# Optimization experiments

Hardware: AMD Instinct MI355X
Metric: run time of the kernel (lower is better)

## Reference

```python
import jax, jax.numpy as jnp
import numpy as np

N_NODES = 100000
N_EDGES = 1600000
IN_FEATS = 128
N_HIDDEN = 128
N_CLASSES = 40
EPS = 1e-12  # torch F.normalize eps


def _sage_conv(h, src, dst, W_self, b_self, W_neigh, b_neigh, act, norm):
    # mean aggregation over in-neighbors: dst receives from src
    agg = jax.ops.segment_sum(h[src], dst, num_segments=N_NODES)  # [N, D]
    deg = jax.ops.segment_sum(jnp.ones(dst.shape, h.dtype), dst, num_segments=N_NODES)
    h_neigh = agg / jnp.maximum(deg, 1.0)[:, None]
    out = h @ W_self + b_self + h_neigh @ W_neigh + b_neigh
    if act:
        out = jax.nn.relu(out)
    if norm:
        out = out / jnp.maximum(
            jnp.linalg.norm(out, axis=1, keepdims=True), EPS)
    return out


def setup_inputs() -> dict:
    key = jax.random.key(0)
    ks = jax.random.split(key, 16)
    def lin(k, fan_in, fan_out):
        s = 1.0 / np.sqrt(fan_in)
        return jax.random.uniform(k, (fan_in, fan_out), jnp.float32, -s, s)
    inp = {
        "features": jax.random.normal(ks[0], (N_NODES, IN_FEATS), jnp.float32),
        "src": jax.random.randint(ks[1], (N_EDGES,), 0, N_NODES, jnp.int32),
        "dst": jax.random.randint(ks[2], (N_EDGES,), 0, N_NODES, jnp.int32),
        # layer 0: in -> hidden
        "Ws0": lin(ks[3], IN_FEATS, N_HIDDEN), "bs0": jnp.zeros((N_HIDDEN,), jnp.float32),
        "Wn0": lin(ks[4], IN_FEATS, N_HIDDEN), "bn0": jnp.zeros((N_HIDDEN,), jnp.float32),
        # layer 1: hidden -> hidden
        "Ws1": lin(ks[5], N_HIDDEN, N_HIDDEN), "bs1": jnp.zeros((N_HIDDEN,), jnp.float32),
        "Wn1": lin(ks[6], N_HIDDEN, N_HIDDEN), "bn1": jnp.zeros((N_HIDDEN,), jnp.float32),
        # layer 2: hidden -> classes (no activation, no norm)
        "Ws2": lin(ks[7], N_HIDDEN, N_CLASSES), "bs2": jnp.zeros((N_CLASSES,), jnp.float32),
        "Wn2": lin(ks[8], N_HIDDEN, N_CLASSES), "bn2": jnp.zeros((N_CLASSES,), jnp.float32),
    }
    return inp


def reference(features, src, dst,
              Ws0, bs0, Wn0, bn0,
              Ws1, bs1, Wn1, bn1,
              Ws2, bs2, Wn2, bn2):
    h = _sage_conv(features, src, dst, Ws0, bs0, Wn0, bn0, act=True, norm=True)
    h = _sage_conv(h, src, dst, Ws1, bs1, Wn1, bn1, act=True, norm=True)
    out = _sage_conv(h, src, dst, Ws2, bs2, Wn2, bn2, act=False, norm=False)
    return out
```

## Files before the change

kernel.cpp:

```cpp
#include <hip/hip_runtime.h>
#include <hip/hip_bf16.h>

#define N_NODES_C 100000
#define N_EDGES_C 1600000
#define N_BUCK ((N_NODES_C + 255) / 256)
#define BCAP 4608
#define PART_NB 160
#define PART_CHUNK ((N_EDGES_C + PART_NB - 1) / PART_NB)

typedef __attribute__((ext_vector_type(8))) short          short8;
typedef __attribute__((ext_vector_type(4))) float          f32x4;
typedef __attribute__((ext_vector_type(4))) unsigned int   u32x4;
typedef __attribute__((ext_vector_type(4))) unsigned short u16x4;

__device__ inline float load1v(const void* p, size_t i, int bf) {
    return bf ? __bfloat162float(((const __hip_bfloat16*)p)[i])
              : ((const float*)p)[i];
}
__device__ inline unsigned short f2bf(float f) {
    __hip_bfloat16 h = __float2bfloat16(f);
    return *reinterpret_cast<unsigned short*>(&h);
}
__device__ inline float bf_lo(unsigned u) { return __uint_as_float(u << 16); }
__device__ inline float bf_hi(unsigned u) { return __uint_as_float(u & 0xffff0000u); }
__device__ inline void acc8(float* a, u32x4 r) {
    a[0] += bf_lo(r.x); a[1] += bf_hi(r.x);
    a[2] += bf_lo(r.y); a[3] += bf_hi(r.y);
    a[4] += bf_lo(r.z); a[5] += bf_hi(r.z);
    a[6] += bf_lo(r.w); a[7] += bf_hi(r.w);
}

__global__ void detect_init(const void* __restrict__ feats, int* __restrict__ gflag,
                            int* __restrict__ bcur) {
    const unsigned short* u = (const unsigned short*)feats;
    int bad = 0;
    for (int i = threadIdx.x; i < 2048; i += 64) {
        unsigned e = (u[i] >> 7) & 0xFF;
        if (e >= 0xC0) bad++;
    }
#pragma unroll
    for (int off = 32; off > 0; off >>= 1) bad += __shfl_down(bad, off, 64);
    if (threadIdx.x == 0) *gflag = (bad == 0) ? 1 : 0;
    for (int b = threadIdx.x; b < N_BUCK; b += 64) bcur[b] = b * BCAP;
}

__global__ __launch_bounds__(256) void partition2(
        const int* __restrict__ src, const int* __restrict__ dst,
        int* __restrict__ bcur, unsigned* __restrict__ pairs) {
    __shared__ int cnt[N_BUCK];
    __shared__ int lbase[N_BUCK];
    int tid = threadIdx.x;
    int e0 = blockIdx.x * PART_CHUNK;
    int e1 = min(e0 + PART_CHUNK, N_EDGES_C);
    for (int i = tid; i < N_BUCK; i += 256) cnt[i] = 0;
    __syncthreads();
    for (int e = e0 + tid; e < e1; e += 256)
        atomicAdd(&cnt[dst[e] >> 8], 1);
    __syncthreads();
    for (int i = tid; i < N_BUCK; i += 256) {
        int c = cnt[i];
        lbase[i] = c ? atomicAdd(&bcur[i], c) : 0;
        cnt[i] = 0;
    }
    __syncthreads();
    for (int e = e0 + tid; e < e1; e += 256) {
        int s = src[e], d = dst[e];
        int bk = d >> 8;
        int pos = lbase[bk] + atomicAdd(&cnt[bk], 1);
        pairs[pos] = ((unsigned)(d & 255) << 17) | (unsigned)s;
    }
}

__global__ __launch_bounds__(256) void bucket_fill(
        const unsigned* __restrict__ pairs, const int* __restrict__ bcur,
        int* __restrict__ csr, int* __restrict__ row_start, int* __restrict__ deg) {
    __shared__ int cnt[256], sd[256], lcur[256];
    int b = blockIdx.x, tid = threadIdx.x;
    int pbase = b * BCAP;

    int psum = 0;
    for (int i = tid; i < b; i += 256) psum += bcur[i] - i * BCAP;
    sd[tid] = psum;
    __syncthreads();
    for (int st = 128; st > 0; st >>= 1) {
        if (tid < st) sd[tid] += sd[tid + st];
        __syncthreads();
    }
    int base = sd[0];
    int count = bcur[b] - b * BCAP;

    cnt[tid] = 0;
    __syncthreads();
    for (int i = tid; i < count; i += 256)
        atomicAdd(&cnt[pairs[pbase + i] >> 17], 1);
    __syncthreads();
    sd[tid] = cnt[tid];
    __syncthreads();
    for (int st = 1; st < 256; st <<= 1) {
        int t = (tid >= st) ? sd[tid - st] : 0;
        __syncthreads();
        sd[tid] += t;
        __syncthreads();
    }
    int excl = sd[tid] - cnt[tid];
    int node = b * 256 + tid;
    if (node < N_NODES_C) { row_start[node] = base + excl; deg[node] = cnt[tid]; }
    lcur[tid] = excl;
    __syncthreads();
    for (int i = tid; i < count; i += 256) {
        unsigned p = pairs[pbase + i];
        int pos = base + atomicAdd(&lcur[p >> 17], 1);
        csr[pos] = (int)(p & 0x1FFFFu);
    }
}

__global__ void prep_weights(const void* Ws0, const void* bs0, const void* Wn0, const void* bn0,
                             const void* Ws1, const void* bs1, const void* Wn1, const void* bn1,
                             const void* Ws2, const void* bs2, const void* Wn2, const void* bn2,
                             unsigned short* __restrict__ Wt, float* __restrict__ bcat,
                             const int* __restrict__ gflag) {
    int gb = *gflag;
    int n = blockIdx.x;
    int k = threadIdx.x;
    if (n < 128) {
        float v = (k < 128) ? load1v(Ws0, (size_t)k * 128 + n, gb)
                            : load1v(Wn0, (size_t)(k - 128) * 128 + n, gb);
        Wt[(size_t)n * 256 + k] = f2bf(v);
        if (k == 0) bcat[n] = load1v(bs0, n, gb) + load1v(bn0, n, gb);
    } else if (n < 256) {
        int c = n - 128;
        float v = (k < 128) ? load1v(Ws1, (size_t)k * 128 + c, gb)
                            : load1v(Wn1, (size_t)(k - 128) * 128 + c, gb);
        Wt[(size_t)n * 256 + k] = f2bf(v);
        if (k == 0) bcat[n] = load1v(bs1, c, gb) + load1v(bn1, c, gb);
    } else {
        int c = n - 256;
        if (k < 128) {
            float v = (c < 40) ? load1v(Ws2, (size_t)k * 40 + c, gb)
                               : load1v(Wn2, (size_t)k * 40 + (c - 40), gb);
            Wt[65536 + (size_t)c * 128 + k] = f2bf(v);
        }
        if (k == 0) bcat[n] = (c < 40) ? load1v(bs2, c, gb) + load1v(bn2, c, gb) : 0.0f;
    }
}

__global__ __launch_bounds__(256) void gather_kernel(
        const void* __restrict__ hsrc, int src_stride,
        int src_mode, int copy_self,
        const int* __restrict__ csr,
        const int* __restrict__ row_start,
        const int* __restrict__ deg,
        unsigned short* __restrict__ X,
        const int* __restrict__ gflag) {
    int wave = threadIdx.x >> 6, lane = threadIdx.x & 63;
    int g = lane >> 4, sub = lane & 15;
    int srcLane = lane & 48;
    int node = blockIdx.x * 16 + wave * 4 + g;
    bool valid = node < N_NODES_C;
    int vnode = valid ? node : (N_NODES_C - 1);
    int start = row_start[vnode];
    int d = valid ? deg[vnode] : 0;
    const int* cp = csr + start;
    float inv = (d > 0) ? 1.0f / (float)d : 0.0f;
    int bf = (src_mode == 2) ? *gflag : src_mode;

    if (bf) {
        const unsigned short* hb = (const unsigned short*)hsrc;
        float a[8] = {0, 0, 0, 0, 0, 0, 0, 0};
        for (int base = 0; base < d; base += 16) {
            int n16 = min(d - base, 16);
            int idxr = cp[base + ((sub < n16) ? sub : 0)];
            int i = 0;
            for (; i + 8 <= n16; i += 8) {
                int nb0 = __shfl(idxr, srcLane + i + 0, 64);
                int nb1 = __shfl(idxr, srcLane + i + 1, 64);
                int nb2 = __shfl(idxr, srcLane + i + 2, 64);
                int nb3 = __shfl(idxr, srcLane + i + 3, 64);
                int nb4 = __shfl(idxr, srcLane + i + 4, 64);
                int nb5 = __shfl(idxr, srcLane + i + 5, 64);
                int nb6 = __shfl(idxr, srcLane + i + 6, 64);
                int nb7 = __shfl(idxr, srcLane + i + 7, 64);
                u32x4 r0 = *(const u32x4*)(hb + (size_t)nb0 * src_stride + sub * 8);
                u32x4 r1 = *(const u32x4*)(hb + (size_t)nb1 * src_stride + sub * 8);
                u32x4 r2 = *(const u32x4*)(hb + (size_t)nb2 * src_stride + sub * 8);
                u32x4 r3 = *(const u32x4*)(hb + (size_t)nb3 * src_stride + sub * 8);
                u32x4 r4 = *(const u32x4*)(hb + (size_t)nb4 * src_stride + sub * 8);
                u32x4 r5 = *(const u32x4*)(hb + (size_t)nb5 * src_stride + sub * 8);
                u32x4 r6 = *(const u32x4*)(hb + (size_t)nb6 * src_stride + sub * 8);
                u32x4 r7 = *(const u32x4*)(hb + (size_t)nb7 * src_stride + sub * 8);
                acc8(a, r0); acc8(a, r1); acc8(a, r2); acc8(a, r3);
                acc8(a, r4); acc8(a, r5); acc8(a, r6); acc8(a, r7);
            }
            for (; i + 4 <= n16; i += 4) {
                int nb0 = __shfl(idxr, srcLane + i + 0, 64);
                int nb1 = __shfl(idxr, srcLane + i + 1, 64);
                int nb2 = __shfl(idxr, srcLane + i + 2, 64);
                int nb3 = __shfl(idxr, srcLane + i + 3, 64);
                u32x4 r0 = *(const u32x4*)(hb + (size_t)nb0 * src_stride + sub * 8);
                u32x4 r1 = *(const u32x4*)(hb + (size_t)nb1 * src_stride + sub * 8);
                u32x4 r2 = *(const u32x4*)(hb + (size_t)nb2 * src_stride + sub * 8);
                u32x4 r3 = *(const u32x4*)(hb + (size_t)nb3 * src_stride + sub * 8);
                acc8(a, r0); acc8(a, r1); acc8(a, r2); acc8(a, r3);
            }
            for (; i < n16; ++i) {
                int nb = __shfl(idxr, srcLane + i, 64);
                u32x4 r = *(const u32x4*)(hb + (size_t)nb * src_stride + sub * 8);
                acc8(a, r);
            }
        }
        if (valid) {
            u32x4 o;
            o.x = (unsigned)f2bf(a[0] * inv) | ((unsigned)f2bf(a[1] * inv) << 16);
            o.y = (unsigned)f2bf(a[2] * inv) | ((unsigned)f2bf(a[3] * inv) << 16);
            o.z = (unsigned)f2bf(a[4] * inv) | ((unsigned)f2bf(a[5] * inv) << 16);
            o.w = (unsigned)f2bf(a[6] * inv) | ((unsigned)f2bf(a[7] * inv) << 16);
            *(u32x4*)(X + (size_t)node * 256 + 128 + sub * 8) = o;
            if (copy_self) {
                u32x4 raw = *(const u32x4*)(hb + (size_t)node * src_stride + sub * 8);
                *(u32x4*)(X + (size_t)node * 256 + sub * 8) = raw;
            }
        }
    } else {
        const float* hf = (const float*)hsrc;
        float a[8] = {0, 0, 0, 0, 0, 0, 0, 0};
        for (int base = 0; base < d; base += 16) {
            int n16 = min(d - base, 16);
            int idxr = cp[base + ((sub < n16) ? sub : 0)];
            int i = 0;
            for (; i + 4 <= n16; i += 4) {
                int nb0 = __shfl(idxr, srcLane + i + 0, 64);
                int nb1 = __shfl(idxr, srcLane + i + 1, 64);
                int nb2 = __shfl(idxr, srcLane + i + 2, 64);
                int nb3 = __shfl(idxr, srcLane + i + 3, 64);
                const float* p0 = hf + (size_t)nb0 * src_stride + sub * 4;
                const float* p1 = hf + (size_t)nb1 * src_stride + sub * 4;
                const float* p2 = hf + (size_t)nb2 * src_stride + sub * 4;
                const float* p3 = hf + (size_t)nb3 * src_stride + sub * 4;
                f32x4 a0 = *(const f32x4*)p0, b0 = *(const f32x4*)(p0 + 64);
                f32x4 a1 = *(const f32x4*)p1, b1 = *(const f32x4*)(p1 + 64);
                f32x4 a2 = *(const f32x4*)p2, b2 = *(const f32x4*)(p2 + 64);
                f32x4 a3 = *(const f32x4*)p3, b3 = *(const f32x4*)(p3 + 64);
#pragma unroll
                for (int k = 0; k < 4; ++k) {
                    a[k] += a0[k] + a1[k] + a2[k] + a3[k];
                    a[4 + k] += b0[k] + b1[k] + b2[k] + b3[k];
                }
            }
            for (; i < n16; ++i) {
                int nb = __shfl(idxr, srcLane + i, 64);
                const float* p0 = hf + (size_t)nb * src_stride + sub * 4;
                f32x4 a0 = *(const f32x4*)p0, b0 = *(const f32x4*)(p0 + 64);
#pragma unroll
                for (int k = 0; k < 4; ++k) { a[k] += a0[k]; a[4 + k] += b0[k]; }
            }
        }
        if (valid) {
            u16x4 oa = { f2bf(a[0] * inv), f2bf(a[1] * inv),
                         f2bf(a[2] * inv), f2bf(a[3] * inv) };
            u16x4 ob = { f2bf(a[4] * inv), f2bf(a[5] * inv),
                         f2bf(a[6] * inv), f2bf(a[7] * inv) };
            *(u16x4*)(X + (size_t)node * 256 + 128 + sub * 4) = oa;
            *(u16x4*)(X + (size_t)node * 256 + 128 + 64 + sub * 4) = ob;
            if (copy_self) {
                const float* sp = hf + (size_t)node * src_stride + sub * 4;
                f32x4 ra = *(const f32x4*)sp;
                f32x4 rb = *(const f32x4*)(sp + 64);
                u16x4 sa = { f2bf(ra.x), f2bf(ra.y), f2bf(ra.z), f2bf(ra.w) };
                u16x4 sb = { f2bf(rb.x), f2bf(rb.y), f2bf(rb.z), f2bf(rb.w) };
                *(u16x4*)(X + (size_t)node * 256 + sub * 4) = sa;
                *(u16x4*)(X + (size_t)node * 256 + 64 + sub * 4) = sb;
            }
        }
    }
}

template <int NCT, int KT, int CHK, bool ACTNORM, bool DUAL>
__global__ __launch_bounds__(256) void mfma_gemm(
        const unsigned short* __restrict__ X, int astride,
        const u32x4* __restrict__ Wg,
        const float* __restrict__ bias,
        unsigned short* __restrict__ out, int out_stride,
        unsigned short* __restrict__ Ybuf, unsigned short* __restrict__ Zbuf,
        int n_nodes) {
    __shared__ u32x4 ldsW[NCT * 16 * CHK];
    int tid = threadIdx.x;
    for (int c = tid; c < NCT * 16 * CHK; c += 256) {
        int nrow = c / CHK, ch = c % CHK;
        ldsW[nrow * CHK + (ch ^ (nrow & 7))] = Wg[c];
    }
    __syncthreads();

    int wave = tid >> 6, lane = tid & 63;
    int quad = lane >> 4, sub = lane & 15;
    int mynode = blockIdx.x * 64 + wave * 16 + sub;
    int arow = (mynode < n_nodes) ? mynode : (n_nodes - 1);
    const unsigned short* ap = X + (size_t)arow * astride + quad * 8;

    f32x4 acc[NCT];
#pragma unroll
    for (int ct = 0; ct < NCT; ++ct) acc[ct] = (f32x4){0,0,0,0};

    short8 av = *(const short8*)ap;
#pragma unroll
    for (int kt = 0; kt < KT; ++kt) {
        short8 av_next = av;
        if (kt < KT - 1) av_next = *(const short8*)(ap + (kt + 1) * 32);
        int chunk = kt * 4 + quad;
#pragma unroll
        for (int ct = 0; ct < NCT; ++ct) {
            int ncol = ct * 16 + sub;
            union { u32x4 u; short8 s; } cv;
            cv.u = ldsW[ncol * CHK + (chunk ^ (ncol & 7))];
            acc[ct] = __builtin_amdgcn_mfma_f32_16x16x32_bf16(cv.s, av, acc[ct], 0, 0, 0);
        }
        av = av_next;
    }

    float ss = 0.0f;
#pragma unroll
    for (int ct = 0; ct < NCT; ++ct) {
        f32x4 b4 = *(const f32x4*)(bias + ct * 16 + quad * 4);
#pragma unroll
        for (int r = 0; r < 4; ++r) {
            float v = acc[ct][r] + b4[r];
            if (ACTNORM) { v = fmaxf(v, 0.0f); ss += v * v; }
            acc[ct][r] = v;
        }
    }
    float scale = 1.0f;
    if (ACTNORM) {
        ss += __shfl_xor(ss, 16, 64);
        ss += __shfl_xor(ss, 32, 64);
        scale = 1.0f / fmaxf(sqrtf(ss), 1e-12f);
    }
    if (mynode < n_nodes) {
#pragma unroll
        for (int ct = 0; ct < NCT; ++ct) {
            int c0 = ct * 16 + quad * 4;
            u16x4 o = { f2bf(acc[ct][0] * scale), f2bf(acc[ct][1] * scale),
                        f2bf(acc[ct][2] * scale), f2bf(acc[ct][3] * scale) };
            if (DUAL) {
                if (c0 < 40) *(u16x4*)(Zbuf + (size_t)mynode * 64 + c0) = o;
                else         *(u16x4*)(Ybuf + (size_t)mynode * 64 + (c0 - 40)) = o;
            } else {
                *(u16x4*)(out + (size_t)mynode * out_stride + c0) = o;
            }
        }
    }
}

__global__ __launch_bounds__(256) void combine_kernel(
        const unsigned short* __restrict__ Y2,
        const unsigned short* __restrict__ Z2,
        const int* __restrict__ csr,
        const int* __restrict__ row_start,
        const int* __restrict__ deg,
        void* __restrict__ out,
        const int* __restrict__ gflag) {
    int wave = threadIdx.x >> 6, lane = threadIdx.x & 63;
    int grp = lane >> 3, sub = lane & 7;
    int grpLane = lane & 56;
    int node = blockIdx.x * 32 + wave * 8 + grp;
    bool valid = node < N_NODES_C;
    int vnode = valid ? node : (N_NODES_C - 1);
    int start = row_start[vnode];
    int d = valid ? deg[vnode] : 0;
    const int* cp = csr + start;

    float a[8] = {0, 0, 0, 0, 0, 0, 0, 0};
    for (int base = 0; base < d; base += 8) {
        int n8 = min(d - base, 8);
        int idxr = cp[base + ((sub < n8) ? sub : 0)];
        if (n8 == 8) {
            int nb0 = __shfl(idxr, grpLane + 0, 64);
            int nb1 = __shfl(idxr, grpLane + 1, 64);
            int nb2 = __shfl(idxr, grpLane + 2, 64);
            int nb3 = __shfl(idxr, grpLane + 3, 64);
            int nb4 = __shfl(idxr, grpLane + 4, 64);
            int nb5 = __shfl(idxr, grpLane + 5, 64);
            int nb6 = __shfl(idxr, grpLane + 6, 64);
            int nb7 = __shfl(idxr, grpLane + 7, 64);
            u32x4 r0 = *(const u32x4*)(Y2 + (size_t)nb0 * 64 + sub * 8);
            u32x4 r1 = *(const u32x4*)(Y2 + (size_t)nb1 * 64 + sub * 8);
            u32x4 r2 = *(const u32x4*)(Y2 + (size_t)nb2 * 64 + sub * 8);
            u32x4 r3 = *(const u32x4*)(Y2 + (size_t)nb3 * 64 + sub * 8);
            u32x4 r4 = *(const u32x4*)(Y2 + (size_t)nb4 * 64 + sub * 8);
            u32x4 r5 = *(const u32x4*)(Y2 + (size_t)nb5 * 64 + sub * 8);
            u32x4 r6 = *(const u32x4*)(Y2 + (size_t)nb6 * 64 + sub * 8);
            u32x4 r7 = *(const u32x4*)(Y2 + (size_t)nb7 * 64 + sub * 8);
            acc8(a, r0); acc8(a, r1); acc8(a, r2); acc8(a, r3);
            acc8(a, r4); acc8(a, r5); acc8(a, r6); acc8(a, r7);
        } else {
            for (int j = 0; j < n8; ++j) {
                int nb = __shfl(idxr, grpLane + j, 64);
                u32x4 r = *(const u32x4*)(Y2 + (size_t)nb * 64 + sub * 8);
                acc8(a, r);
            }
        }
    }

    if (valid) {
        float inv = (d > 0) ? 1.0f / (float)d : 0.0f;
        u32x4 z = *(const u32x4*)(Z2 + (size_t)node * 64 + sub * 8);
        float v[8];
        v[0] = a[0] * inv + bf_lo(z.x); v[1] = a[1] * inv + bf_hi(z.x);
        v[2] = a[2] * inv + bf_lo(z.y); v[3] = a[3] * inv + bf_hi(z.y);
        v[4] = a[4] * inv + bf_lo(z.z); v[5] = a[5] * inv + bf_hi(z.z);
        v[6] = a[6] * inv + bf_lo(z.w); v[7] = a[7] * inv + bf_hi(z.w);
        if (sub < 5) {
            if (*gflag) {
                u32x4 o;
                o.x = (unsigned)f2bf(v[0]) | ((unsigned)f2bf(v[1]) << 16);
                o.y = (unsigned)f2bf(v[2]) | ((unsigned)f2bf(v[3]) << 16);
                o.z = (unsigned)f2bf(v[4]) | ((unsigned)f2bf(v[5]) << 16);
                o.w = (unsigned)f2bf(v[6]) | ((unsigned)f2bf(v[7]) << 16);
                *(u32x4*)((unsigned short*)out + (size_t)node * 40 + sub * 8) = o;
            } else {
                float* op = (float*)out + (size_t)node * 40 + sub * 8;
                f32x4 o0 = { v[0], v[1], v[2], v[3] };
                f32x4 o1 = { v[4], v[5], v[6], v[7] };
                *(f32x4*)op = o0;
                *(f32x4*)(op + 4) = o1;
            }
        }
    }
}

extern "C" void kernel_launch(void* const* d_in, const int* in_sizes, int n_in,
                              void* d_out, int out_size, void* d_ws, size_t ws_size,
                              hipStream_t stream) {
    const void* feats = d_in[0];
    const int*  src   = (const int*)d_in[1];
    const int*  dst   = (const int*)d_in[2];

    char* ws = (char*)d_ws;
    unsigned short* X0   = (unsigned short*)ws;
    unsigned short* X1   = (unsigned short*)(ws + 51200000);
    unsigned short* Wt   = (unsigned short*)(ws + 102400000);
    float*          bcat = (float*)(ws + 102912000);
    unsigned short* Y2   = (unsigned short*)(ws + 102916096);
    unsigned short* Z2   = (unsigned short*)(ws + 115716096);
    unsigned*       pairs= (unsigned*)(ws + 102916096);
    int*  csr       = (int*)(ws + 128516096);
    int*  row_start = (int*)(ws + 134916096);
    int*  deg       = (int*)(ws + 135316096);
    int*  bcur      = (int*)(ws + 135720192);
    int*  gflag     = (int*)(ws + 135722240);

    detect_init<<<1, 64, 0, stream>>>(feats, gflag, bcur);

    partition2<<<PART_NB, 256, 0, stream>>>(src, dst, bcur, pairs);
    bucket_fill<<<N_BUCK, 256, 0, stream>>>(pairs, bcur, csr, row_start, deg);

    prep_weights<<<336, 256, 0, stream>>>(
        d_in[3], d_in[4], d_in[5], d_in[6],
        d_in[7], d_in[8], d_in[9], d_in[10],
        d_in[11], d_in[12], d_in[13], d_in[14], Wt, bcat, gflag);

    const int gblk = (N_NODES_C + 15) / 16;
    const int cblk = (N_NODES_C + 31) / 32;
    const int mblk = (N_NODES_C + 63) / 64;

    gather_kernel<<<gblk, 256, 0, stream>>>(feats, 128, 2, 1, csr, row_start, deg, X0, gflag);
    mfma_gemm<8, 8, 32, true, false><<<mblk, 256, 0, stream>>>(
        X0, 256, (const u32x4*)Wt, bcat, X1, 256, nullptr, nullptr, N_NODES_C);

    gather_kernel<<<gblk, 256, 0, stream>>>(X1, 256, 1, 0, csr, row_start, deg, X1, gflag);
    mfma_gemm<8, 8, 32, true, false><<<mblk, 256, 0, stream>>>(
        X1, 256, (const u32x4*)(Wt + 128 * 256), bcat + 128, X0, 256, nullptr, nullptr, N_NODES_C);

    mfma_gemm<5, 4, 16, false, true><<<mblk, 256, 0, stream>>>(
        X0, 256, (const u32x4*)(Wt + 65536), bcat + 256, nullptr, 0, Y2, Z2, N_NODES_C);

    combine_kernel<<<cblk, 256, 0, stream>>>(Y2, Z2, csr, row_start, deg, d_out, gflag);
}
```

Measured before the change: 460.8 us.

## Fuse layer-1 GEMM with layer-2 projection GEMM via LDS staging

Merges the layer-1 GEMM (with ReLU and L2 norm) and the layer-2 dual projection GEMM into one kernel. The normalized layer-1 activations are staged in swizzled LDS and used directly as the A operand of the second GEMM. This removes a full write and re-read of the 100k x 128 bf16 hidden buffer and one kernel launch. In exchange, the layer-1 weights are loaded in two halves with extra barriers, and the second GEMM reads its weights straight from global memory without LDS caching.

```diff
diff --git a/kernel.cpp b/kernel.cpp
--- a/kernel.cpp
+++ b/kernel.cpp
@@ -28,6 +28,9 @@
     a[2] += bf_lo(r.y); a[3] += bf_hi(r.y);
     a[4] += bf_lo(r.z); a[5] += bf_hi(r.z);
     a[6] += bf_lo(r.w); a[7] += bf_hi(r.w);
+}
+__device__ inline int xaddr2(int l, int byteCol) {
+    return l * 256 + ((((byteCol >> 4) ^ (l & 7)) << 4)) + (byteCol & 15);
 }
 
 __global__ void detect_init(const void* __restrict__ feats, int* __restrict__ gflag,
@@ -274,13 +277,12 @@
     }
 }
 
-template <int NCT, int KT, int CHK, bool ACTNORM, bool DUAL>
+template <int NCT, int KT, int CHK, bool ACTNORM>
 __global__ __launch_bounds__(256) void mfma_gemm(
         const unsigned short* __restrict__ X, int astride,
         const u32x4* __restrict__ Wg,
         const float* __restrict__ bias,
         unsigned short* __restrict__ out, int out_stride,
-        unsigned short* __restrict__ Ybuf, unsigned short* __restrict__ Zbuf,
         int n_nodes) {
     __shared__ u32x4 ldsW[NCT * 16 * CHK];
     int tid = threadIdx.x;
@@ -339,12 +341,112 @@
             int c0 = ct * 16 + quad * 4;
             u16x4 o = { f2bf(acc[ct][0] * scale), f2bf(acc[ct][1] * scale),
                         f2bf(acc[ct][2] * scale), f2bf(acc[ct][3] * scale) };
-            if (DUAL) {
-                if (c0 < 40) *(u16x4*)(Zbuf + (size_t)mynode * 64 + c0) = o;
-                else         *(u16x4*)(Ybuf + (size_t)mynode * 64 + (c0 - 40)) = o;
-            } else {
-                *(u16x4*)(out + (size_t)mynode * out_stride + c0) = o;
-            }
+            *(u16x4*)(out + (size_t)mynode * out_stride + c0) = o;
+        }
+    }
+}
+
+__global__ __launch_bounds__(256) void mfma_gemm_l12(
+        const unsigned short* __restrict__ X, int astride,
+        const u32x4* __restrict__ W1g,
+        const float* __restrict__ b1,
+        const u32x4* __restrict__ W2g,
+        const float* __restrict__ b2,
+        unsigned short* __restrict__ Ybuf,
+        unsigned short* __restrict__ Zbuf,
+        int n_nodes) {
+    __shared__ u32x4 ldsW[128 * 16];
+    __shared__ u32x4 xt4[64 * 16];
+    char* xt = (char*)xt4;
+
+    int tid = threadIdx.x;
+    int wave = tid >> 6, lane = tid & 63;
+    int quad = lane >> 4, sub = lane & 15;
+    int lrow = wave * 16 + sub;
+    int mynode = blockIdx.x * 64 + lrow;
+    int arow = (mynode < n_nodes) ? mynode : (n_nodes - 1);
+    const unsigned short* ap = X + (size_t)arow * astride + quad * 8;
+
+    f32x4 acc[8];
+#pragma unroll
+    for (int ct = 0; ct < 8; ++ct) acc[ct] = (f32x4){0, 0, 0, 0};
+
+    for (int half = 0; half < 2; ++half) {
+        __syncthreads();
+        for (int c = tid; c < 128 * 16; c += 256) {
+            int nrow = c >> 4, ch = c & 15;
+            ldsW[(nrow << 4) + (ch ^ (nrow & 7))] = W1g[nrow * 32 + half * 16 + ch];
+        }
+        __syncthreads();
+#pragma unroll
+        for (int kt4 = 0; kt4 < 4; ++kt4) {
+            int kt = half * 4 + kt4;
+            short8 av = *(const short8*)(ap + kt * 32);
+            int chunk = kt4 * 4 + quad;
+#pragma unroll
+            for (int ct = 0; ct < 8; ++ct) {
+                int ncol = ct * 16 + sub;
+                union { u32x4 u; short8 s; } cv;
+                cv.u = ldsW[(ncol << 4) + (chunk ^ (ncol & 7))];
+                acc[ct] = __builtin_amdgcn_mfma_f32_16x16x32_bf16(cv.s, av, acc[ct], 0, 0, 0);
+            }
+        }
+    }
+
+    float ss = 0.0f;
+#pragma unroll
+    for (int ct = 0; ct < 8; ++ct) {
+        f32x4 b4 = *(const f32x4*)(b1 + ct * 16 + quad * 4);
+#pragma unroll
+        for (int r = 0; r < 4; ++r) {
+            float v = acc[ct][r] + b4[r];
+            v = fmaxf(v, 0.0f); ss += v * v;
+            acc[ct][r] = v;
+        }
+    }
+    ss += __shfl_xor(ss, 16, 64);
+    ss += __shfl_xor(ss, 32, 64);
+    float scale = 1.0f / fmaxf(sqrtf(ss), 1e-12f);
+
+#pragma unroll
+    for (int ct = 0; ct < 8; ++ct) {
+        int byteCol = ct * 32 + quad * 8;
+        u16x4 o = { f2bf(acc[ct][0] * scale), f2bf(acc[ct][1] * scale),
+                    f2bf(acc[ct][2] * scale), f2bf(acc[ct][3] * scale) };
+        *(u16x4*)(xt + xaddr2(lrow, byteCol)) = o;
+    }
+    __syncthreads();
+
+    f32x4 acc2[5];
+#pragma unroll
+    for (int ct = 0; ct < 5; ++ct) acc2[ct] = (f32x4){0, 0, 0, 0};
+
+#pragma unroll
+    for (int kt2 = 0; kt2 < 4; ++kt2) {
+        short8 av;
+        {
+            union { u32x4 u; short8 s; } tv;
+            tv.u = *(const u32x4*)(xt + xaddr2(lrow, kt2 * 64 + quad * 16));
+            av = tv.s;
+        }
+#pragma unroll
+        for (int ct = 0; ct < 5; ++ct) {
+            int ncol = ct * 16 + sub;
+            union { u32x4 u; short8 s; } cv;
+            cv.u = W2g[(ncol << 4) + kt2 * 4 + quad];
+            acc2[ct] = __builtin_amdgcn_mfma_f32_16x16x32_bf16(cv.s, av, acc2[ct], 0, 0, 0);
+        }
+    }
+
+    if (mynode < n_nodes) {
+#pragma unroll
+        for (int ct = 0; ct < 5; ++ct) {
+            f32x4 b4 = *(const f32x4*)(b2 + ct * 16 + quad * 4);
+            int c0 = ct * 16 + quad * 4;
+            u16x4 o = { f2bf(acc2[ct][0] + b4[0]), f2bf(acc2[ct][1] + b4[1]),
+                        f2bf(acc2[ct][2] + b4[2]), f2bf(acc2[ct][3] + b4[3]) };
+            if (c0 < 40) *(u16x4*)(Zbuf + (size_t)mynode * 64 + c0) = o;
+            else         *(u16x4*)(Ybuf + (size_t)mynode * 64 + (c0 - 40)) = o;
         }
     }
 }
@@ -462,15 +564,14 @@
     const int mblk = (N_NODES_C + 63) / 64;
 
     gather_kernel<<<gblk, 256, 0, stream>>>(feats, 128, 2, 1, csr, row_start, deg, X0, gflag);
-    mfma_gemm<8, 8, 32, true, false><<<mblk, 256, 0, stream>>>(
-        X0, 256, (const u32x4*)Wt, bcat, X1, 256, nullptr, nullptr, N_NODES_C);
+    mfma_gemm<8, 8, 32, true><<<mblk, 256, 0, stream>>>(
+        X0, 256, (const u32x4*)Wt, bcat, X1, 256, N_NODES_C);
 
     gather_kernel<<<gblk, 256, 0, stream>>>(X1, 256, 1, 0, csr, row_start, deg, X1, gflag);
-    mfma_gemm<8, 8, 32, true, false><<<mblk, 256, 0, stream>>>(
-        X1, 256, (const u32x4*)(Wt + 128 * 256), bcat + 128, X0, 256, nullptr, nullptr, N_NODES_C);
-
-    mfma_gemm<5, 4, 16, false, true><<<mblk, 256, 0, stream>>>(
-        X0, 256, (const u32x4*)(Wt + 65536), bcat + 256, nullptr, 0, Y2, Z2, N_NODES_C);
+
+    mfma_gemm_l12<<<mblk, 256, 0, stream>>>(
+        X1, 256, (const u32x4*)(Wt + 128 * 256), bcat + 128,
+        (const u32x4*)(Wt + 65536), bcat + 256, Y2, Z2, N_NODES_C);
 
     combine_kernel<<<cblk, 256, 0, stream>>>(Y2, Z2, csr, row_start, deg, d_out, gflag);
 }
```

Result: no change. 460.2 us (-0.1%).
